# Kernel optimization log

Hardware: AMD Instinct MI355X
Metric: run time of the kernel (lower is better)

The kernel has to match this reference:

```python
import jax, jax.numpy as jnp
import numpy as np

E, I, H, T = 8, 2816, 1024, 8192

def setup_inputs() -> dict:
    key = jax.random.key(0)
    ks = jax.random.split(key, 5)
    scale_w = 1.0 / np.sqrt(H)
    return {
        "hidden_states": jax.random.normal(ks[0], (T, H), jnp.float32),
        "router_logits": jax.random.normal(ks[1], (T, E), jnp.float32),
        "W1": jax.random.normal(ks[2], (E, I, H), jnp.float32) * scale_w,
        "W3": jax.random.normal(ks[3], (E, I, H), jnp.float32) * scale_w,
        "W2": jax.random.normal(ks[4], (E, H, I), jnp.float32) * (1.0 / np.sqrt(I)),
        "top_k": 2,
    }

def reference(hidden_states, router_logits, W1, W3, W2, top_k):
    # softmax router in fp32, topk, renormalize (renormalize=True, use_grouped_topk=False)
    probs = jax.nn.softmax(router_logits.astype(jnp.float32), axis=-1)  # [T,E]
    vals, idx = jax.lax.top_k(probs, top_k)                             # [T,K]
    vals = vals / jnp.sum(vals, axis=-1, keepdims=True)
    vals = vals.astype(hidden_states.dtype)
    n_tok, n_exp = probs.shape
    # dense per-token expert weight matrix [T,E]; zero for unrouted experts,
    # mathematically identical to the gather/scatter-add in the ipex op
    w = jnp.zeros((n_tok, n_exp), hidden_states.dtype).at[
        jnp.arange(n_tok)[:, None], idx].add(vals)

    def expert_step(acc, args):
        We1, We3, We2, we = args  # [I,H], [I,H], [H,I], [T]
        h = jax.nn.silu(hidden_states @ We1.T) * (hidden_states @ We3.T)  # [T,I]
        return acc + we[:, None] * (h @ We2.T), None

    out, _ = jax.lax.scan(expert_step, jnp.zeros_like(hidden_states),
                          (W1, W3, W2, w.T))
    return out
```

## Files before the change

### kernel.cpp

```cpp
#include <hip/hip_runtime.h>
#include <stdint.h>

#define NE 8
#define NI 2816
#define NH 1024
#define NT 8192
#define NPAIR (NT * 2)

typedef __bf16 bf16x8 __attribute__((ext_vector_type(8)));
typedef float f32x4 __attribute__((ext_vector_type(4)));

__device__ __forceinline__ uint16_t f2bf(float f) {
    union { float f; uint32_t u; } v;
    v.f = f;
    return (uint16_t)((v.u + 0x7FFFu + ((v.u >> 16) & 1u)) >> 16);
}

__device__ __forceinline__ void gld16(const void* g, void* l) {
    __builtin_amdgcn_global_load_lds(
        (__attribute__((address_space(1))) void*)(uintptr_t)g,
        (__attribute__((address_space(3))) void*)(uint32_t)(uintptr_t)l,
        16, 0, 0);
}

__global__ __launch_bounds__(256) void k_cvt(const float* __restrict__ s,
                                             uint16_t* __restrict__ d, int n8) {
    int i = blockIdx.x * 256 + threadIdx.x;
    if (i >= n8) return;
    float4 a = ((const float4*)s)[(size_t)i * 2];
    float4 b = ((const float4*)s)[(size_t)i * 2 + 1];
    uint4 o;
    o.x = (uint32_t)f2bf(a.x) | ((uint32_t)f2bf(a.y) << 16);
    o.y = (uint32_t)f2bf(a.z) | ((uint32_t)f2bf(a.w) << 16);
    o.z = (uint32_t)f2bf(b.x) | ((uint32_t)f2bf(b.y) << 16);
    o.w = (uint32_t)f2bf(b.z) | ((uint32_t)f2bf(b.w) << 16);
    ((uint4*)d)[i] = o;
}

__global__ __launch_bounds__(256) void k_router(const float* __restrict__ logits,
                                                int* __restrict__ tok_e,
                                                float2* __restrict__ tok_w,
                                                int* __restrict__ counts) {
    int t = blockIdx.x * 256 + threadIdx.x;
    if (t >= NT) return;
    float4 a = ((const float4*)logits)[(size_t)t * 2];
    float4 b = ((const float4*)logits)[(size_t)t * 2 + 1];
    float l[8] = {a.x, a.y, a.z, a.w, b.x, b.y, b.z, b.w};
    int i0 = 0; float l0 = l[0];
#pragma unroll
    for (int e = 1; e < 8; e++) if (l[e] > l0) { l0 = l[e]; i0 = e; }
    int i1 = -1; float l1 = -3.4e38f;
#pragma unroll
    for (int e = 0; e < 8; e++) if (e != i0 && l[e] > l1) { l1 = l[e]; i1 = e; }
    float w0 = 1.f / (1.f + __expf(l1 - l0));
    float w1 = 1.f - w0;
    tok_e[t] = i0 | (i1 << 8);
    tok_w[t] = make_float2(w0, w1);
    atomicAdd(&counts[i0], 1);
    atomicAdd(&counts[i1], 1);
}

__global__ void k_scan(const int* __restrict__ counts, int* __restrict__ offsets,
                       int* __restrict__ cursor) {
    if (threadIdx.x == 0) {
        int o = 0;
        for (int e = 0; e < NE; e++) { offsets[e] = o; cursor[e] = o; o += counts[e]; }
    }
}

__global__ __launch_bounds__(128) void k_gather(const float* __restrict__ x,
                                                const int* __restrict__ tok_e,
                                                const float2* __restrict__ tok_w,
                                                int* __restrict__ cursor,
                                                uint16_t* __restrict__ Xg,
                                                int* __restrict__ slot_tok,
                                                float* __restrict__ slot_w) {
    int t = blockIdx.x;
    __shared__ int ss[2];
    if (threadIdx.x == 0) {
        int ee = tok_e[t];
        float2 w = tok_w[t];
        int s0 = atomicAdd(&cursor[ee & 0xff], 1);
        int s1 = atomicAdd(&cursor[(ee >> 8) & 0xff], 1);
        ss[0] = s0; ss[1] = s1;
        slot_tok[s0] = t; slot_w[s0] = w.x;
        slot_tok[s1] = t; slot_w[s1] = w.y;
    }
    __syncthreads();
    int s0 = ss[0], s1 = ss[1];
    int i = threadIdx.x;
    const float4* xr = (const float4*)(x + (size_t)t * NH);
    float4 a = xr[i * 2];
    float4 b = xr[i * 2 + 1];
    uint4 o;
    o.x = (uint32_t)f2bf(a.x) | ((uint32_t)f2bf(a.y) << 16);
    o.y = (uint32_t)f2bf(a.z) | ((uint32_t)f2bf(a.w) << 16);
    o.z = (uint32_t)f2bf(b.x) | ((uint32_t)f2bf(b.y) << 16);
    o.w = (uint32_t)f2bf(b.z) | ((uint32_t)f2bf(b.w) << 16);
    ((uint4*)(Xg + (size_t)s0 * NH))[i] = o;
    ((uint4*)(Xg + (size_t)s1 * NH))[i] = o;
}

__global__ __launch_bounds__(256, 2) void k_gemm1(const uint16_t* __restrict__ Xg,
                                                  const uint16_t* __restrict__ W1b,
                                                  const uint16_t* __restrict__ W3b,
                                                  uint16_t* __restrict__ Hbuf,
                                                  const int* __restrict__ counts,
                                                  const int* __restrict__ offsets) {
    int e = blockIdx.z;
    int n_e = counts[e];
    int mtile = blockIdx.y;
    if (mtile * 128 >= n_e) return;
    int ntile = blockIdx.x;
    int off = offsets[e];

    __shared__ __align__(16) uint16_t As[128 * 32];
    __shared__ __align__(16) uint16_t B1s[128 * 32];
    __shared__ __align__(16) uint16_t B3s[128 * 32];

    int tid = threadIdx.x;
    int r = tid >> 2, c = tid & 3;
    int wv = tid >> 6, lane = tid & 63;
    int wr = wv >> 1, wc = wv & 1;
    int m_in = lane & 15, q = lane >> 4;

    int rowA0 = off + mtile * 128 + r;
    int rowA1 = min(rowA0 + 64, NPAIR - 1);
    rowA0 = min(rowA0, NPAIR - 1);
    const uint16_t* a0 = Xg + (size_t)rowA0 * NH + c * 8;
    const uint16_t* a1 = Xg + (size_t)rowA1 * NH + c * 8;
    const uint16_t* b1r = W1b + ((size_t)e * NI + ntile * 128 + r) * NH + c * 8;
    const uint16_t* b3r = W3b + ((size_t)e * NI + ntile * 128 + r) * NH + c * 8;

    uint16_t* lA0 = &As[tid * 8];   uint16_t* lA1 = &As[2048 + tid * 8];
    uint16_t* lB10 = &B1s[tid * 8]; uint16_t* lB11 = &B1s[2048 + tid * 8];
    uint16_t* lB30 = &B3s[tid * 8]; uint16_t* lB31 = &B3s[2048 + tid * 8];

    const uint16_t* pa = &As[(wr * 64 + m_in) * 32 + q * 8];
    const uint16_t* pb1 = &B1s[(wc * 64 + m_in) * 32 + q * 8];
    const uint16_t* pb3 = &B3s[(wc * 64 + m_in) * 32 + q * 8];

    f32x4 acc1[4][4] = {};
    f32x4 acc3[4][4] = {};

    for (int k0 = 0; k0 < NH; k0 += 32) {
        gld16(a0 + k0, lA0);
        gld16(a1 + k0, lA1);
        gld16(b1r + k0, lB10);
        gld16(b1r + (size_t)64 * NH + k0, lB11);
        gld16(b3r + k0, lB30);
        gld16(b3r + (size_t)64 * NH + k0, lB31);
        __syncthreads();

        bf16x8 af[4], b1f[4], b3f[4];
#pragma unroll
        for (int it = 0; it < 4; it++) af[it] = *(const bf16x8*)(pa + it * 512);
#pragma unroll
        for (int jt = 0; jt < 4; jt++) {
            b1f[jt] = *(const bf16x8*)(pb1 + jt * 512);
            b3f[jt] = *(const bf16x8*)(pb3 + jt * 512);
        }
#pragma unroll
        for (int it = 0; it < 4; it++)
#pragma unroll
            for (int jt = 0; jt < 4; jt++) {
                acc1[it][jt] = __builtin_amdgcn_mfma_f32_16x16x32_bf16(af[it], b1f[jt], acc1[it][jt], 0, 0, 0);
                acc3[it][jt] = __builtin_amdgcn_mfma_f32_16x16x32_bf16(af[it], b3f[jt], acc3[it][jt], 0, 0, 0);
            }
        __syncthreads();
    }

    int sBase = off + mtile * 128;
#pragma unroll
    for (int it = 0; it < 4; it++) {
#pragma unroll
        for (int reg = 0; reg < 4; reg++) {
            int lm = wr * 64 + it * 16 + q * 4 + reg;
            if (mtile * 128 + lm < n_e) {
                uint16_t* orow = Hbuf + (size_t)(sBase + lm) * NI + ntile * 128 + wc * 64 + m_in;
#pragma unroll
                for (int jt = 0; jt < 4; jt++) {
                    float c1 = acc1[it][jt][reg];
                    float c3 = acc3[it][jt][reg];
                    float hv = (c1 / (1.f + __expf(-c1))) * c3;
                    orow[jt * 16] = f2bf(hv);
                }
            }
        }
    }
}

__global__ __launch_bounds__(256, 2) void k_gemm2(const uint16_t* __restrict__ Hbuf,
                                                  const uint16_t* __restrict__ W2b,
                                                  float* __restrict__ out,
                                                  const int* __restrict__ counts,
                                                  const int* __restrict__ offsets,
                                                  const int* __restrict__ slot_tok,
                                                  const float* __restrict__ slot_w) {
    int e = blockIdx.z;
    int n_e = counts[e];
    int mtile = blockIdx.y;
    if (mtile * 128 >= n_e) return;
    int ntile = blockIdx.x;
    int off = offsets[e];

    __shared__ __align__(16) uint16_t As[128 * 32];
    __shared__ __align__(16) uint16_t Bs[128 * 32];

    int tid = threadIdx.x;
    int r = tid >> 2, c = tid & 3;
    int wv = tid >> 6, lane = tid & 63;
    int wr = wv >> 1, wc = wv & 1;
    int m_in = lane & 15, q = lane >> 4;

    int rowA0 = off + mtile * 128 + r;
    int rowA1 = min(rowA0 + 64, NPAIR - 1);
    rowA0 = min(rowA0, NPAIR - 1);
    const uint16_t* a0 = Hbuf + (size_t)rowA0 * NI + c * 8;
    const uint16_t* a1 = Hbuf + (size_t)rowA1 * NI + c * 8;
    const uint16_t* br = W2b + ((size_t)e * NH + ntile * 128 + r) * NI + c * 8;

    uint16_t* lA0 = &As[tid * 8]; uint16_t* lA1 = &As[2048 + tid * 8];
    uint16_t* lB0 = &Bs[tid * 8]; uint16_t* lB1 = &Bs[2048 + tid * 8];

    const uint16_t* pa = &As[(wr * 64 + m_in) * 32 + q * 8];
    const uint16_t* pb = &Bs[(wc * 64 + m_in) * 32 + q * 8];

    f32x4 acc[4][4] = {};

    for (int k0 = 0; k0 < NI; k0 += 32) {
        gld16(a0 + k0, lA0);
        gld16(a1 + k0, lA1);
        gld16(br + k0, lB0);
        gld16(br + (size_t)64 * NI + k0, lB1);
        __syncthreads();

        bf16x8 af[4], bf[4];
#pragma unroll
        for (int it = 0; it < 4; it++) af[it] = *(const bf16x8*)(pa + it * 512);
#pragma unroll
        for (int jt = 0; jt < 4; jt++) bf[jt] = *(const bf16x8*)(pb + jt * 512);
#pragma unroll
        for (int it = 0; it < 4; it++)
#pragma unroll
            for (int jt = 0; jt < 4; jt++)
                acc[it][jt] = __builtin_amdgcn_mfma_f32_16x16x32_bf16(af[it], bf[jt], acc[it][jt], 0, 0, 0);
        __syncthreads();
    }

    int sBase = off + mtile * 128;
#pragma unroll
    for (int it = 0; it < 4; it++) {
#pragma unroll
        for (int reg = 0; reg < 4; reg++) {
            int lm = wr * 64 + it * 16 + q * 4 + reg;
            if (mtile * 128 + lm < n_e) {
                int slot = sBase + lm;
                int tk = slot_tok[slot];
                float w = slot_w[slot];
                float* orow = out + (size_t)tk * NH + ntile * 128 + wc * 64 + m_in;
#pragma unroll
                for (int jt = 0; jt < 4; jt++) {
#if defined(__HIP_DEVICE_COMPILE__)
                    unsafeAtomicAdd(&orow[jt * 16], acc[it][jt][reg] * w);
#else
                    atomicAdd(&orow[jt * 16], acc[it][jt][reg] * w);
#endif
                }
            }
        }
    }
}

extern "C" void kernel_launch(void* const* d_in, const int* in_sizes, int n_in,
                              void* d_out, int out_size, void* d_ws, size_t ws_size,
                              hipStream_t stream) {
    const float* x = (const float*)d_in[0];
    const float* logits = (const float*)d_in[1];
    const float* W1 = (const float*)d_in[2];
    const float* W3 = (const float*)d_in[3];
    const float* W2 = (const float*)d_in[4];
    float* out = (float*)d_out;

    char* ws = (char*)d_ws;
    size_t o = 0;
    auto nxt = [&](size_t b) -> void* {
        void* p = ws + o;
        o += (b + 255) & ~(size_t)255;
        return p;
    };
    const size_t WELEMS = (size_t)NE * NI * NH;
    uint16_t* W1b = (uint16_t*)nxt(WELEMS * 2);
    uint16_t* W3b = (uint16_t*)nxt(WELEMS * 2);
    uint16_t* W2b = (uint16_t*)nxt(WELEMS * 2);
    uint16_t* Xg = (uint16_t*)nxt((size_t)NPAIR * NH * 2);
    uint16_t* Hbuf = (uint16_t*)nxt((size_t)NPAIR * NI * 2);
    int* slot_tok = (int*)nxt((size_t)NPAIR * 4);
    float* slot_w = (float*)nxt((size_t)NPAIR * 4);
    int* tok_e = (int*)nxt((size_t)NT * 4);
    float2* tok_w = (float2*)nxt((size_t)NT * 8);
    int* meta = (int*)nxt(128);
    int* counts = meta;
    int* offsets = meta + 8;
    int* cursor = meta + 16;
    (void)ws_size; (void)in_sizes; (void)n_in;

    hipMemsetAsync(meta, 0, 128, stream);
    hipMemsetAsync(d_out, 0, (size_t)out_size * sizeof(float), stream);

    k_router<<<NT / 256, 256, 0, stream>>>(logits, tok_e, tok_w, counts);
    k_scan<<<1, 64, 0, stream>>>(counts, offsets, cursor);

    int n8 = (int)(WELEMS / 8);
    k_cvt<<<n8 / 256, 256, 0, stream>>>(W1, W1b, n8);
    k_cvt<<<n8 / 256, 256, 0, stream>>>(W3, W3b, n8);
    k_cvt<<<n8 / 256, 256, 0, stream>>>(W2, W2b, n8);

    k_gather<<<NT, 128, 0, stream>>>(x, tok_e, tok_w, cursor, Xg, slot_tok, slot_w);

    k_gemm1<<<dim3(NI / 128, NT / 128, NE), 256, 0, stream>>>(Xg, W1b, W3b, Hbuf, counts, offsets);
    k_gemm2<<<dim3(NH / 128, NT / 128, NE), 256, 0, stream>>>(Hbuf, W2b, out, counts, offsets, slot_tok, slot_w);
}
```

Baseline: 981.7 us.

## Replace gemm2 atomic scatter with bf16 expert output buffer and combine kernel

Result: faster. 961.0 us (-2.1%).

```diff
diff --git a/kernel.cpp b/kernel.cpp
--- a/kernel.cpp
+++ b/kernel.cpp
@@ -16,6 +16,13 @@
     return (uint16_t)((v.u + 0x7FFFu + ((v.u >> 16) & 1u)) >> 16);
 }
 
+__device__ __forceinline__ float bflo(uint32_t u) {
+    union { uint32_t x; float f; } v; v.x = u << 16; return v.f;
+}
+__device__ __forceinline__ float bfhi(uint32_t u) {
+    union { uint32_t x; float f; } v; v.x = u & 0xffff0000u; return v.f;
+}
+
 __device__ __forceinline__ void gld16(const void* g, void* l) {
     __builtin_amdgcn_global_load_lds(
         (__attribute__((address_space(1))) void*)(uintptr_t)g,
@@ -23,10 +30,15 @@
         16, 0, 0);
 }
 
-__global__ __launch_bounds__(256) void k_cvt(const float* __restrict__ s,
-                                             uint16_t* __restrict__ d, int n8) {
+__global__ __launch_bounds__(256) void k_cvt3(const float* __restrict__ W1,
+                                              const float* __restrict__ W3,
+                                              const float* __restrict__ W2,
+                                              uint16_t* __restrict__ W1b,
+                                              uint16_t* __restrict__ W3b,
+                                              uint16_t* __restrict__ W2b) {
     int i = blockIdx.x * 256 + threadIdx.x;
-    if (i >= n8) return;
+    const float* s = blockIdx.y == 0 ? W1 : (blockIdx.y == 1 ? W3 : W2);
+    uint16_t* d = blockIdx.y == 0 ? W1b : (blockIdx.y == 1 ? W3b : W2b);
     float4 a = ((const float4*)s)[(size_t)i * 2];
     float4 b = ((const float4*)s)[(size_t)i * 2 + 1];
     uint4 o;
@@ -73,7 +85,7 @@
                                                 const float2* __restrict__ tok_w,
                                                 int* __restrict__ cursor,
                                                 uint16_t* __restrict__ Xg,
-                                                int* __restrict__ slot_tok,
+                                                int2* __restrict__ tok_slots,
                                                 float* __restrict__ slot_w) {
     int t = blockIdx.x;
     __shared__ int ss[2];
@@ -83,8 +95,9 @@
         int s0 = atomicAdd(&cursor[ee & 0xff], 1);
         int s1 = atomicAdd(&cursor[(ee >> 8) & 0xff], 1);
         ss[0] = s0; ss[1] = s1;
-        slot_tok[s0] = t; slot_w[s0] = w.x;
-        slot_tok[s1] = t; slot_w[s1] = w.y;
+        tok_slots[t] = make_int2(s0, s1);
+        slot_w[s0] = w.x;
+        slot_w[s1] = w.y;
     }
     __syncthreads();
     int s0 = ss[0], s1 = ss[1];
@@ -192,11 +205,9 @@
 
 __global__ __launch_bounds__(256, 2) void k_gemm2(const uint16_t* __restrict__ Hbuf,
                                                   const uint16_t* __restrict__ W2b,
-                                                  float* __restrict__ out,
+                                                  uint16_t* __restrict__ Ybuf,
                                                   const int* __restrict__ counts,
-                                                  const int* __restrict__ offsets,
-                                                  const int* __restrict__ slot_tok,
-                                                  const float* __restrict__ slot_w) {
+                                                  const int* __restrict__ offsets) {
     int e = blockIdx.z;
     int n_e = counts[e];
     int mtile = blockIdx.y;
@@ -255,21 +266,38 @@
         for (int reg = 0; reg < 4; reg++) {
             int lm = wr * 64 + it * 16 + q * 4 + reg;
             if (mtile * 128 + lm < n_e) {
-                int slot = sBase + lm;
-                int tk = slot_tok[slot];
-                float w = slot_w[slot];
-                float* orow = out + (size_t)tk * NH + ntile * 128 + wc * 64 + m_in;
-#pragma unroll
-                for (int jt = 0; jt < 4; jt++) {
-#if defined(__HIP_DEVICE_COMPILE__)
-                    unsafeAtomicAdd(&orow[jt * 16], acc[it][jt][reg] * w);
-#else
-                    atomicAdd(&orow[jt * 16], acc[it][jt][reg] * w);
-#endif
-                }
+                uint16_t* orow = Ybuf + (size_t)(sBase + lm) * NH + ntile * 128 + wc * 64 + m_in;
+#pragma unroll
+                for (int jt = 0; jt < 4; jt++)
+                    orow[jt * 16] = f2bf(acc[it][jt][reg]);
             }
         }
     }
+}
+
+__global__ __launch_bounds__(256) void k_combine(const uint16_t* __restrict__ Y,
+                                                 const int2* __restrict__ tok_slots,
+                                                 const float* __restrict__ slot_w,
+                                                 float* __restrict__ out) {
+    int idx = blockIdx.x * 256 + threadIdx.x;
+    int t = idx >> 7;
+    int g = idx & 127;
+    int2 s = tok_slots[t];
+    float w0 = slot_w[s.x], w1 = slot_w[s.y];
+    uint4 u0 = ((const uint4*)(Y + (size_t)s.x * NH))[g];
+    uint4 u1 = ((const uint4*)(Y + (size_t)s.y * NH))[g];
+    float4 o0, o1;
+    o0.x = w0 * bflo(u0.x) + w1 * bflo(u1.x);
+    o0.y = w0 * bfhi(u0.x) + w1 * bfhi(u1.x);
+    o0.z = w0 * bflo(u0.y) + w1 * bflo(u1.y);
+    o0.w = w0 * bfhi(u0.y) + w1 * bfhi(u1.y);
+    o1.x = w0 * bflo(u0.z) + w1 * bflo(u1.z);
+    o1.y = w0 * bfhi(u0.z) + w1 * bfhi(u1.z);
+    o1.z = w0 * bflo(u0.w) + w1 * bflo(u1.w);
+    o1.w = w0 * bfhi(u0.w) + w1 * bfhi(u1.w);
+    float4* orow = (float4*)(out + (size_t)t * NH + g * 8);
+    orow[0] = o0;
+    orow[1] = o1;
 }
 
 extern "C" void kernel_launch(void* const* d_in, const int* in_sizes, int n_in,
@@ -295,29 +323,27 @@
     uint16_t* W2b = (uint16_t*)nxt(WELEMS * 2);
     uint16_t* Xg = (uint16_t*)nxt((size_t)NPAIR * NH * 2);
     uint16_t* Hbuf = (uint16_t*)nxt((size_t)NPAIR * NI * 2);
-    int* slot_tok = (int*)nxt((size_t)NPAIR * 4);
     float* slot_w = (float*)nxt((size_t)NPAIR * 4);
+    int2* tok_slots = (int2*)nxt((size_t)NT * 8);
     int* tok_e = (int*)nxt((size_t)NT * 4);
     float2* tok_w = (float2*)nxt((size_t)NT * 8);
     int* meta = (int*)nxt(128);
     int* counts = meta;
     int* offsets = meta + 8;
     int* cursor = meta + 16;
+    uint16_t* Ybuf = Xg;
     (void)ws_size; (void)in_sizes; (void)n_in;
 
     hipMemsetAsync(meta, 0, 128, stream);
-    hipMemsetAsync(d_out, 0, (size_t)out_size * sizeof(float), stream);
 
     k_router<<<NT / 256, 256, 0, stream>>>(logits, tok_e, tok_w, counts);
     k_scan<<<1, 64, 0, stream>>>(counts, offsets, cursor);
 
-    int n8 = (int)(WELEMS / 8);
-    k_cvt<<<n8 / 256, 256, 0, stream>>>(W1, W1b, n8);
-    k_cvt<<<n8 / 256, 256, 0, stream>>>(W3, W3b, n8);
-    k_cvt<<<n8 / 256, 256, 0, stream>>>(W2, W2b, n8);
-
-    k_gather<<<NT, 128, 0, stream>>>(x, tok_e, tok_w, cursor, Xg, slot_tok, slot_w);
+    k_cvt3<<<dim3((unsigned)(WELEMS / 8 / 256), 3), 256, 0, stream>>>(W1, W3, W2, W1b, W3b, W2b);
+
+    k_gather<<<NT, 128, 0, stream>>>(x, tok_e, tok_w, cursor, Xg, tok_slots, slot_w);
 
     k_gemm1<<<dim3(NI / 128, NT / 128, NE), 256, 0, stream>>>(Xg, W1b, W3b, Hbuf, counts, offsets);
-    k_gemm2<<<dim3(NH / 128, NT / 128, NE), 256, 0, stream>>>(Hbuf, W2b, out, counts, offsets, slot_tok, slot_w);
-}
+    k_gemm2<<<dim3(NH / 128, NT / 128, NE), 256, 0, stream>>>(Hbuf, W2b, Ybuf, counts, offsets);
+    k_combine<<<NT * NH / 8 / 256, 256, 0, stream>>>(Ybuf, tok_slots, slot_w, out);
+}
```
